# Kernel optimization log

Measured on AMD Instinct MI355X. Metric: run time of the kernel, lower is better.

## Reference

```python
import jax, jax.numpy as jnp
import numpy as np

EPS = 1e-5
MIN_NORM = 1e-10

def _norm(x):
    return jnp.sqrt(jnp.clip(jnp.sum(x * x, axis=-1, keepdims=True), MIN_NORM, None))

def _proj(x):
    # clip points to the open unit Poincare ball
    n = _norm(x)
    max_n = 1.0 - EPS
    return jnp.where(n > max_n, x * (max_n / n), x)

def _artanh(x):
    return jnp.arctanh(jnp.clip(x, -1.0 + EPS, 1.0 - EPS))

def mob_add(u, v):
    uv = jnp.sum(u * v, axis=-1, keepdims=True)
    u2 = jnp.sum(u * u, axis=-1, keepdims=True)
    v2 = jnp.sum(v * v, axis=-1, keepdims=True)
    num = (1.0 + 2.0 * uv + v2) * u + (1.0 - u2) * v
    den = 1.0 + 2.0 * uv + u2 * v2
    return _proj(num / jnp.maximum(den, MIN_NORM))

def mob_mat_mul(M, x):
    # M: [Din, Dout], x: [B, Din] on the ball. Ganea Mobius matvec.
    x = _proj(x)
    Mx = x @ M
    x_n = _norm(x)
    Mx_n = _norm(Mx)
    return _proj(jnp.tanh(Mx_n / x_n * _artanh(x_n)) * (Mx / Mx_n))

def log_map_zero(y):
    n = _norm(y)
    return _artanh(n) * y / n

def exp_map_zero(v):
    n = _norm(v)
    return _proj(jnp.tanh(n) * v / n)

def mob_pointwise_prod(x, u):
    # coordinate-wise scale of hyperbolic x by gate u, in the tangent space at 0
    return exp_map_zero(log_map_zero(x) * u)

def _transition(W, h, U, x, b):
    Wh = mob_mat_mul(W, h)
    Ux = mob_mat_mul(U, x)
    return mob_add(mob_add(Wh, Ux), b)

def setup_inputs() -> dict:
    B, I, H = 2048, 1024, 1024
    Din, Dh = 2 * I, 2 * H
    k = (1.0 / H) ** 0.5
    key = jax.random.key(0)
    ks = jax.random.split(key, 8)
    return {
        "hyp_x": jax.random.normal(ks[0], (B, Din), jnp.float32) * 0.01,
        "hidden": jax.random.normal(ks[1], (B, Dh), jnp.float32) * 0.01,
        "w_z": jax.random.uniform(ks[2], (Dh, Dh), jnp.float32, -k, k),
        "w_r": jax.random.uniform(ks[3], (Dh, Dh), jnp.float32, -k, k),
        "w_h": jax.random.uniform(ks[4], (Dh, Dh), jnp.float32, -k, k),
        "u_z": jax.random.uniform(ks[5], (Din, Dh), jnp.float32, -k, k),
        "u_r": jax.random.uniform(ks[6], (Din, Dh), jnp.float32, -k, k),
        "b_z": jnp.zeros((Dh,), jnp.float32),
        "b_r": jnp.zeros((Dh,), jnp.float32),
        "b_h": jnp.zeros((Dh,), jnp.float32),
    }

def reference(hyp_x, hidden, w_z, w_r, w_h, u_z, u_r, b_z, b_r, b_h):
    hyp_x = _proj(hyp_x)
    hidden = _proj(hidden)
    z = jax.nn.sigmoid(log_map_zero(_transition(w_z, hidden, u_z, hyp_x, b_z)))
    r = jax.nn.sigmoid(log_map_zero(_transition(w_r, hidden, u_r, hyp_x, b_r)))
    r_point_h = mob_pointwise_prod(hidden, r)
    # NOTE: original source uses u_r (not u_h) here; replicated faithfully.
    h_tilde = _transition(w_h, r_point_h, u_r, hyp_x, b_h)
    minus_h_oplus_htilde = mob_add(-hidden, h_tilde)
    new_h = mob_add(hidden, mob_pointwise_prod(minus_h_oplus_htilde, z))
    return new_h
```

## Files before the change

### kernel.cpp

```cpp
#include <hip/hip_runtime.h>
#include <hip/hip_bf16.h>
#include <math.h>

#define EPS 1e-5f
#define MAXN (1.0f - EPS)
#define MINN 1e-10f

constexpr int D = 2048;

typedef unsigned short u16;
typedef __bf16 bf16x8 __attribute__((ext_vector_type(8)));
typedef float floatx4 __attribute__((ext_vector_type(4)));


__device__ __forceinline__ u16 f2bf(float f) {
    union { float f; unsigned u; } v; v.f = f;
    unsigned r = v.u + 0x7FFFu + ((v.u >> 16) & 1u);
    return (u16)(r >> 16);
}

__device__ __forceinline__ float bf2f(u16 b) {
    union { unsigned u; float f; } v; v.u = ((unsigned)b) << 16; return v.f;
}

__device__ __forceinline__ void load_bf8(const u16* p, float* d) {
    uint4 r = *(const uint4*)p;
    unsigned w[4] = {r.x, r.y, r.z, r.w};
    #pragma unroll
    for (int i = 0; i < 4; ++i) {
        d[2 * i]     = bf2f((u16)(w[i] & 0xFFFFu));
        d[2 * i + 1] = bf2f((u16)(w[i] >> 16));
    }
}

__device__ __forceinline__ void store_bf8(u16* p, const float* s) {
    u16 pk[8];
    #pragma unroll
    for (int i = 0; i < 8; ++i) pk[i] = f2bf(s[i]);
    *(uint4*)p = *(const uint4*)pk;
}

__device__ __forceinline__ void load_f8(const float* p, float* d) {
    *(float4*)(d)     = *(const float4*)(p);
    *(float4*)(d + 4) = *(const float4*)(p + 4);
}

__device__ __forceinline__ void store_f8(float* p, const float* s) {
    *(float4*)(p)     = *(const float4*)(s);
    *(float4*)(p + 4) = *(const float4*)(s + 4);
}

__device__ __forceinline__ float artanh_(float x) {
    x = fminf(fmaxf(x, -1.0f + EPS), 1.0f - EPS);
    return 0.5f * logf((1.0f + x) / (1.0f - x));
}

__device__ __forceinline__ float sigmoid_(float x) {
    return 1.0f / (1.0f + expf(-x));
}

__device__ __forceinline__ void gl_lds16(const u16* g, u16* l) {
    __builtin_amdgcn_global_load_lds(
        (const __attribute__((address_space(1))) unsigned int*)g,
        (__attribute__((address_space(3))) unsigned int*)l, 16, 0, 0);
}

template<int N>
__device__ __forceinline__ void block_sums(float* v, float* sbuf) {
    #pragma unroll
    for (int n = 0; n < N; ++n)
        #pragma unroll
        for (int off = 32; off >= 1; off >>= 1) v[n] += __shfl_xor(v[n], off, 64);
    int w = threadIdx.x >> 6;
    __syncthreads();
    if ((threadIdx.x & 63) == 0) {
        #pragma unroll
        for (int n = 0; n < N; ++n) sbuf[w * N + n] = v[n];
    }
    __syncthreads();
    #pragma unroll
    for (int n = 0; n < N; ++n)
        v[n] = sbuf[n] + sbuf[N + n] + sbuf[2 * N + n] + sbuf[3 * N + n];
}

__device__ __forceinline__ void mmm_finish(float sum2, float g, float* coef, float* onorm) {
    float mxn = sqrtf(fmaxf(sum2, MINN));
    float tt  = tanhf(mxn * g);
    float on  = fminf(tt, MAXN);
    *coef = on / mxn;
    *onorm = on;
}

__device__ __forceinline__ float mob_apply(float* u, const float* v,
                                           float u2, float v2, float duv) {
    float cu  = 1.f + 2.f * duv + v2;
    float cv  = 1.f - u2;
    float den = fmaxf(1.f + 2.f * duv + u2 * v2, MINN);
    float s2  = cu * cu * u2 + 2.f * cu * cv * duv + cv * cv * v2;
    float n   = sqrtf(fmaxf(s2 / (den * den), MINN));
    float sc  = ((n > MAXN) ? MAXN / n : 1.f) / den;
    #pragma unroll
    for (int i = 0; i < 8; ++i) u[i] = sc * (cu * u[i] + cv * v[i]);
    return fminf(n, MAXN);
}

__device__ __forceinline__ void trans_tile(const float* W, u16* Wt,
                                           int n0, int k0, float* tile) {
    int t = threadIdx.x;
    int lr = t >> 4, lc = (t & 15) * 4;
    #pragma unroll
    for (int p = 0; p < 4; ++p) {
        int r = lr + p * 16;
        float4 v = *(const float4*)(W + (size_t)(k0 + r) * D + n0 + lc);
        tile[r * 65 + lc + 0] = v.x;
        tile[r * 65 + lc + 1] = v.y;
        tile[r * 65 + lc + 2] = v.z;
        tile[r * 65 + lc + 3] = v.w;
    }
    __syncthreads();
    int wn = t >> 3, ws = (t & 7) * 8;
    #pragma unroll
    for (int p = 0; p < 2; ++p) {
        int n = wn + p * 32;
        u16 pk[8];
        #pragma unroll
        for (int j = 0; j < 8; ++j) pk[j] = f2bf(tile[(ws + j) * 65 + n]);
        *(uint4*)(Wt + (size_t)(n0 + n) * D + k0 + ws) = *(uint4*)pk;
    }
}


struct PrepBatch {
    const float* W[5]; u16* Wt[5];
    const float* hx; const float* h;
    u16* hx_bf; u16* h_bf;
    float* g_x; float* g_h;
};

__global__ __launch_bounds__(256) void wtrans_prep(PrepBatch pb) {
    __shared__ float tile[64 * 65];
    int t = threadIdx.x;

    if (blockIdx.z != 4) {
        int wi = (blockIdx.z == 5) ? 4 : blockIdx.z;
        trans_tile(pb.W[wi], pb.Wt[wi],
                   blockIdx.x * 64, blockIdx.y * 64, tile);
    } else {
        int bid = blockIdx.y * (D / 64) + blockIdx.x;
        for (int rr = 0; rr < 2; ++rr) {
            int b = bid * 2 + rr;
            size_t off = (size_t)b * D + t * 8;
            float xv[8], hv[8];
            load_f8(pb.hx + off, xv);
            load_f8(pb.h + off, hv);
            float s[2] = {0.f, 0.f};
            #pragma unroll
            for (int i = 0; i < 8; ++i) { s[0] += xv[i] * xv[i]; s[1] += hv[i] * hv[i]; }
            block_sums<2>(s, tile);

            float nx = sqrtf(fmaxf(s[0], MINN));
            float scx = (nx > MAXN) ? MAXN / nx : 1.0f;
            float nh = sqrtf(fmaxf(s[1], MINN));
            float sch = (nh > MAXN) ? MAXN / nh : 1.0f;
            #pragma unroll
            for (int i = 0; i < 8; ++i) { xv[i] *= scx; hv[i] *= sch; }
            store_bf8(pb.hx_bf + off, xv);
            store_bf8(pb.h_bf + off, hv);
            if (t == 0) {
                float xn = fminf(nx, MAXN), hn = fminf(nh, MAXN);
                pb.g_x[b] = artanh_(xn) / xn;
                pb.g_h[b] = artanh_(hn) / hn;
            }
        }
    }
}


#define PHASE_MID() do { \
    __builtin_amdgcn_s_barrier(); \
    asm volatile("s_waitcnt lgkmcnt(0)" ::: "memory"); \
    __builtin_amdgcn_sched_barrier(0); \
    __builtin_amdgcn_s_setprio(1); } while (0)

#define PHASE_END() do { \
    __builtin_amdgcn_s_setprio(0); \
    __builtin_amdgcn_s_barrier(); } while (0)

template<int KLEN, int NJ>
__device__ __forceinline__ void gemm256_body(const u16* __restrict__ A,
                                             const u16* __restrict__ W,
                                             u16* __restrict__ C, int koff,
                                             u16* As, u16* Ws) {
    constexpr int T  = KLEN / 64;
    constexpr int BN = NJ * 64;
    constexpr int AU = 8192;
    constexpr int BU = BN * 32;

    int t0 = threadIdx.x;
    int wave = t0 >> 6, lane = t0 & 63, l16 = lane & 15, quad = lane >> 4;
    int wr = wave >> 2, wc = wave & 3;
    int brow = blockIdx.y * 256, bcol = blockIdx.x * BN;

    int srow = t0 >> 2;
    int sseg = (t0 & 3) ^ ((srow >> 1) & 3);
    const u16* srcA = A + (size_t)(brow + srow) * D + koff + sseg * 8;
    const u16* srcB = W + (size_t)(bcol + srow) * D + koff + sseg * 8;
    u16* ldsA = As + wave * 512;
    u16* ldsB = Ws + wave * 512;

    auto stageA = [&](int buf, int kh, int tile) {
        const u16* s = srcA + tile * 64 + kh * 32;
        u16* d = ldsA + (buf * 2 + kh) * AU;
        gl_lds16(s, d);
        gl_lds16(s + (size_t)128 * D, d + 4096);
    };
    auto stageB = [&](int buf, int kh, int tile) {
        const u16* s = srcB + tile * 64 + kh * 32;
        u16* d = ldsB + (buf * 2 + kh) * BU;
        gl_lds16(s, d);
        if constexpr (NJ == 4) gl_lds16(s + (size_t)128 * D, d + 4096);
    };

    const u16* aF = As + (wr * 128 + l16) * 32 + ((quad ^ ((l16 >> 1) & 3)) * 8);
    const u16* bF = Ws + (wc * (NJ * 16) + l16) * 32 + ((quad ^ ((l16 >> 1) & 3)) * 8);

    floatx4 acc[8][NJ];
    #pragma unroll
    for (int i = 0; i < 8; ++i)
        #pragma unroll
        for (int j = 0; j < NJ; ++j)
            #pragma unroll
            for (int e = 0; e < 4; ++e) acc[i][j][e] = 0.f;

    stageA(0, 0, 0); stageB(0, 0, 0);
    stageA(0, 1, 0); stageB(0, 1, 0);
    stageA(1, 0, 1); stageB(1, 0, 1);
    if constexpr (NJ == 4) asm volatile("s_waitcnt vmcnt(4)" ::: "memory");
    else                   asm volatile("s_waitcnt vmcnt(3)" ::: "memory");
    __builtin_amdgcn_s_barrier();

    #pragma unroll 2
    for (int tt = 0; tt < T; ++tt) {
        int bsel = tt & 1, bno = bsel ^ 1;
        const u16* aT = aF + bsel * (2 * AU);
        const u16* bT = bF + bsel * (2 * BU);
        bool st1 = (tt + 1) < T, st2 = (tt + 2) < T;

        if constexpr (NJ == 4) {
            bf16x8 bfr[4], afr[4];
            #pragma unroll
            for (int j = 0; j < 4; ++j) bfr[j] = *(const bf16x8*)(bT + j * 512);
            #pragma unroll
            for (int i = 0; i < 4; ++i) afr[i] = *(const bf16x8*)(aT + i * 512);
            if (st1) stageA(bno, 1, tt + 1);
            PHASE_MID();
            #pragma unroll
            for (int i = 0; i < 4; ++i)
                #pragma unroll
                for (int j = 0; j < 4; ++j)
                    acc[i][j] = __builtin_amdgcn_mfma_f32_16x16x32_bf16(afr[i], bfr[j], acc[i][j], 0, 0, 0);
            PHASE_END();
            #pragma unroll
            for (int i = 0; i < 4; ++i) afr[i] = *(const bf16x8*)(aT + (4 + i) * 512);
            if (st1) stageB(bno, 1, tt + 1);
            PHASE_MID();
            #pragma unroll
            for (int i = 0; i < 4; ++i)
                #pragma unroll
                for (int j = 0; j < 4; ++j)
                    acc[4 + i][j] = __builtin_amdgcn_mfma_f32_16x16x32_bf16(afr[i], bfr[j], acc[4 + i][j], 0, 0, 0);
            PHASE_END();
            #pragma unroll
            for (int j = 0; j < 4; ++j) bfr[j] = *(const bf16x8*)(bT + BU + j * 512);
            #pragma unroll
            for (int i = 0; i < 4; ++i) afr[i] = *(const bf16x8*)(aT + AU + i * 512);
            if (st2) stageA(bsel, 0, tt + 2);
            PHASE_MID();
            #pragma unroll
            for (int i = 0; i < 4; ++i)
                #pragma unroll
                for (int j = 0; j < 4; ++j)
                    acc[i][j] = __builtin_amdgcn_mfma_f32_16x16x32_bf16(afr[i], bfr[j], acc[i][j], 0, 0, 0);
            PHASE_END();
            #pragma unroll
            for (int i = 0; i < 4; ++i) afr[i] = *(const bf16x8*)(aT + AU + (4 + i) * 512);
            if (st2) stageB(bsel, 0, tt + 2);
            PHASE_MID();
            #pragma unroll
            for (int i = 0; i < 4; ++i)
                #pragma unroll
                for (int j = 0; j < 4; ++j)
                    acc[4 + i][j] = __builtin_amdgcn_mfma_f32_16x16x32_bf16(afr[i], bfr[j], acc[4 + i][j], 0, 0, 0);
            __builtin_amdgcn_s_setprio(0);
            asm volatile("s_waitcnt vmcnt(4)" ::: "memory");
            __builtin_amdgcn_s_barrier();
        } else {
            bf16x8 bfr[2], afr[8];
            #pragma unroll
            for (int j = 0; j < 2; ++j) bfr[j] = *(const bf16x8*)(bT + j * 512);
            #pragma unroll
            for (int i = 0; i < 8; ++i) afr[i] = *(const bf16x8*)(aT + i * 512);
            if (st1) { stageA(bno, 1, tt + 1); stageB(bno, 1, tt + 1); }
            PHASE_MID();
            #pragma unroll
            for (int i = 0; i < 8; ++i)
                #pragma unroll
                for (int j = 0; j < 2; ++j)
                    acc[i][j] = __builtin_amdgcn_mfma_f32_16x16x32_bf16(afr[i], bfr[j], acc[i][j], 0, 0, 0);
            PHASE_END();
            #pragma unroll
            for (int j = 0; j < 2; ++j) bfr[j] = *(const bf16x8*)(bT + BU + j * 512);
            #pragma unroll
            for (int i = 0; i < 8; ++i) afr[i] = *(const bf16x8*)(aT + AU + i * 512);
            if (st2) { stageA(bsel, 0, tt + 2); stageB(bsel, 0, tt + 2); }
            PHASE_MID();
            #pragma unroll
            for (int i = 0; i < 8; ++i)
                #pragma unroll
                for (int j = 0; j < 2; ++j)
                    acc[i][j] = __builtin_amdgcn_mfma_f32_16x16x32_bf16(afr[i], bfr[j], acc[i][j], 0, 0, 0);
            __builtin_amdgcn_s_setprio(0);
            asm volatile("s_waitcnt vmcnt(3)" ::: "memory");
            __builtin_amdgcn_s_barrier();
        }
    }

    #pragma unroll
    for (int i = 0; i < 8; ++i) {
        #pragma unroll
        for (int j = 0; j < NJ; ++j) {
            int row = brow + wr * 128 + i * 16 + quad * 4;
            int col = bcol + wc * (NJ * 16) + j * 16 + l16;
            #pragma unroll
            for (int r = 0; r < 4; ++r)
                C[(size_t)(row + r) * D + col] = f2bf(acc[i][j][r]);
        }
    }
}


struct G1Batch { const u16* A[4]; const u16* W[4]; u16* C[4]; };

__global__ __launch_bounds__(512, 2) void g1_kernel(G1Batch gb) {
    __shared__ u16 As[32768];
    __shared__ u16 Ws[32768];
    int z = blockIdx.z;
    gemm256_body<2048, 4>(gb.A[z], gb.W[z], gb.C[z], 0, As, Ws);
}


struct GemmBatch { const u16* A[2]; const u16* W[2]; u16* C[2]; int koff[2]; };

__global__ __launch_bounds__(512, 2) void g2_kernel(GemmBatch gb) {
    __shared__ u16 As[32768];
    __shared__ u16 Ws[16384];
    int z = blockIdx.z;
    gemm256_body<1024, 2>(gb.A[z], gb.W[z], gb.C[z], gb.koff[z], As, Ws);
}


__global__ __launch_bounds__(256) void mid_kernel(
    const u16* __restrict__ c_wz, const u16* __restrict__ c_uz,
    const u16* __restrict__ c_wr, const u16* __restrict__ c_ur,
    const u16* __restrict__ h_bf,
    const float* __restrict__ g_x, const float* __restrict__ g_h,
    const float* __restrict__ b_z, const float* __restrict__ b_r,
    u16* __restrict__ z_out, u16* __restrict__ uxr_out,
    u16* __restrict__ rph_bf, float* __restrict__ g_rph) {
    __shared__ float sbuf[24];
    int b = blockIdx.x, t = threadIdx.x;
    size_t off = (size_t)b * D + t * 8;
    int cbase = t * 8;

    float wz[8], uz[8], wr2[8], ur2[8], hp[8], bz[8], br[8];
    load_bf8(c_wz + off, wz);
    load_bf8(c_uz + off, uz);
    load_bf8(c_wr + off, wr2);
    load_bf8(c_ur + off, ur2);
    load_bf8(h_bf + off, hp);
    load_f8(b_z + cbase, bz);
    load_f8(b_r + cbase, br);

    float s[6] = {0, 0, 0, 0, 0, 0};
    #pragma unroll
    for (int i = 0; i < 8; ++i) {
        s[0] += wz[i] * wz[i];  s[1] += uz[i] * uz[i];
        s[2] += wr2[i] * wr2[i]; s[3] += ur2[i] * ur2[i];
        s[4] += bz[i] * bz[i];  s[5] += br[i] * br[i];
    }
    block_sums<6>(s, sbuf);
    float gh = g_h[b], gx = g_x[b];

    float cwz, nwz, cuz, nuz, cwr, nwr, cur, nur;
    mmm_finish(s[0], gh, &cwz, &nwz);
    mmm_finish(s[1], gx, &cuz, &nuz);
    mmm_finish(s[2], gh, &cwr, &nwr);
    mmm_finish(s[3], gx, &cur, &nur);
    #pragma unroll
    for (int i = 0; i < 8; ++i) {
        wz[i] *= cwz; uz[i] *= cuz; wr2[i] *= cwr; ur2[i] *= cur;
    }
    float sbz = s[4], sbr2 = s[5];

    float d[2] = {0.f, 0.f};
    #pragma unroll
    for (int i = 0; i < 8; ++i) { d[0] += wz[i] * uz[i]; d[1] += wr2[i] * ur2[i]; }
    block_sums<2>(d, sbuf);
    float n1z = mob_apply(wz, uz, nwz * nwz, nuz * nuz, d[0]);
    float n1r = mob_apply(wr2, ur2, nwr * nwr, nur * nur, d[1]);

    d[0] = 0.f; d[1] = 0.f;
    #pragma unroll
    for (int i = 0; i < 8; ++i) { d[0] += wz[i] * bz[i]; d[1] += wr2[i] * br[i]; }
    block_sums<2>(d, sbuf);
    float n2z = mob_apply(wz, bz, n1z * n1z, sbz, d[0]);
    float n2r = mob_apply(wr2, br, n1r * n1r, sbr2, d[1]);

    float gz = artanh_(n2z) / n2z;
    float gr = artanh_(n2r) / n2r;
    float zz[8], v[8];
    float sv = 0.f;
    #pragma unroll
    for (int i = 0; i < 8; ++i) {
        zz[i] = sigmoid_(gz * wz[i]);
        float r = sigmoid_(gr * wr2[i]);
        v[i] = gh * hp[i] * r;
        sv += v[i] * v[i];
    }
    store_bf8(z_out + off, zz);
    block_sums<1>(&sv, sbuf);
    float nv = sqrtf(fmaxf(sv, MINN));
    float th = fminf(tanhf(nv), MAXN);
    float cr = th / nv;
    #pragma unroll
    for (int i = 0; i < 8; ++i) v[i] *= cr;
    store_bf8(rph_bf + off, v);
    store_bf8(uxr_out + off, ur2);
    if (t == 0) g_rph[b] = artanh_(th) / th;
}


__global__ __launch_bounds__(256) void fin_kernel(
    const u16* __restrict__ p0, const u16* __restrict__ p1,
    const u16* __restrict__ uxr, const u16* __restrict__ z_in,
    const u16* __restrict__ h_bf,
    const float* __restrict__ g_rph, const float* __restrict__ b_h,
    float* __restrict__ out) {
    __shared__ float sbuf[16];
    int b = blockIdx.x, t = threadIdx.x;
    size_t off = (size_t)b * D + t * 8;
    int cbase = t * 8;

    float wh[8], ux[8], zz[8], hp[8], bh[8], t0[8];
    load_bf8(p0 + off, wh);
    load_bf8(p1 + off, t0);
    #pragma unroll
    for (int i = 0; i < 8; ++i) wh[i] += t0[i];
    load_bf8(uxr + off, ux);
    load_bf8(z_in + off, zz);
    load_bf8(h_bf + off, hp);
    load_f8(b_h + cbase, bh);

    float s[4] = {0, 0, 0, 0};
    #pragma unroll
    for (int i = 0; i < 8; ++i) {
        s[0] += wh[i] * wh[i]; s[1] += ux[i] * ux[i];
        s[2] += hp[i] * hp[i]; s[3] += bh[i] * bh[i];
    }
    block_sums<4>(s, sbuf);
    float swh = s[0], sux = s[1], shp = s[2], sbh = s[3];

    float cwh, nwh;
    mmm_finish(swh, g_rph[b], &cwh, &nwh);
    #pragma unroll
    for (int i = 0; i < 8; ++i) wh[i] *= cwh;

    float d = 0.f;
    #pragma unroll
    for (int i = 0; i < 8; ++i) d += wh[i] * ux[i];
    block_sums<1>(&d, sbuf);
    float n1 = mob_apply(wh, ux, nwh * nwh, sux, d);

    d = 0.f;
    #pragma unroll
    for (int i = 0; i < 8; ++i) d += wh[i] * bh[i];
    block_sums<1>(&d, sbuf);
    float nht = mob_apply(wh, bh, n1 * n1, sbh, d);

    #pragma unroll
    for (int i = 0; i < 8; ++i) ux[i] = -hp[i];
    d = 0.f;
    #pragma unroll
    for (int i = 0; i < 8; ++i) d += ux[i] * wh[i];
    block_sums<1>(&d, sbuf);
    float nm = mob_apply(ux, wh, shp, nht * nht, d);

    float lm = artanh_(nm) / nm;
    float sv = 0.f;
    #pragma unroll
    for (int i = 0; i < 8; ++i) {
        float v = lm * ux[i] * zz[i];
        ux[i] = v;
        sv += v * v;
    }
    block_sums<1>(&sv, sbuf);
    float nv = sqrtf(fmaxf(sv, MINN));
    float th = fminf(tanhf(nv), MAXN);
    float ce = th / nv;
    #pragma unroll
    for (int i = 0; i < 8; ++i) ux[i] *= ce;

    d = 0.f;
    #pragma unroll
    for (int i = 0; i < 8; ++i) d += hp[i] * ux[i];
    block_sums<1>(&d, sbuf);
    mob_apply(hp, ux, shp, th * th, d);
    store_f8(out + off, hp);
}


extern "C" void kernel_launch(void* const* d_in, const int* in_sizes, int n_in,
                              void* d_out, int out_size, void* d_ws, size_t ws_size,
                              hipStream_t stream) {
    const float* hyp_x  = (const float*)d_in[0];
    const float* hidden = (const float*)d_in[1];
    const float* w_z = (const float*)d_in[2];
    const float* w_r = (const float*)d_in[3];
    const float* w_h = (const float*)d_in[4];
    const float* u_z = (const float*)d_in[5];
    const float* u_r = (const float*)d_in[6];
    const float* b_z = (const float*)d_in[7];
    const float* b_r = (const float*)d_in[8];
    const float* b_h = (const float*)d_in[9];
    float* out = (float*)d_out;

    int B = in_sizes[1] / D;

    char* ws = (char*)d_ws;
    size_t o = 0;
    auto alloc = [&](size_t bytes) -> void* {
        void* p = ws + o;
        o += (bytes + 255) & ~(size_t)255;
        return p;
    };
    u16* wt[5];
    for (int i = 0; i < 5; ++i) wt[i] = (u16*)alloc((size_t)D * D * 2);
    u16* hx_bf = (u16*)alloc((size_t)B * D * 2);
    u16* h_bf  = (u16*)alloc((size_t)B * D * 2);
    float* g_x   = (float*)alloc((size_t)B * 4);
    float* g_h   = (float*)alloc((size_t)B * 4);
    float* g_rph = (float*)alloc((size_t)B * 4);
    u16* cz0 = (u16*)alloc((size_t)B * D * 2);
    u16* cz1 = (u16*)alloc((size_t)B * D * 2);
    u16* cz2 = (u16*)alloc((size_t)B * D * 2);
    u16* cz3 = (u16*)alloc((size_t)B * D * 2);
    u16* p0 = (u16*)alloc((size_t)B * D * 2);
    u16* p1 = (u16*)alloc((size_t)B * D * 2);
    u16* z_buf = (u16*)alloc((size_t)B * D * 2);
    u16* uxr = (u16*)alloc((size_t)B * D * 2);
    u16* rph = (u16*)alloc((size_t)B * D * 2);

    PrepBatch pb;
    pb.W[0] = w_z; pb.Wt[0] = wt[0];
    pb.W[1] = w_r; pb.Wt[1] = wt[1];
    pb.W[2] = u_z; pb.Wt[2] = wt[3];
    pb.W[3] = u_r; pb.Wt[3] = wt[4];
    pb.W[4] = w_h; pb.Wt[4] = wt[2];
    pb.hx = hyp_x; pb.h = hidden;
    pb.hx_bf = hx_bf; pb.h_bf = h_bf;
    pb.g_x = g_x; pb.g_h = g_h;
    wtrans_prep<<<dim3(D / 64, D / 64, 6), 256, 0, stream>>>(pb);

    G1Batch g1;
    g1.A[0] = h_bf;  g1.W[0] = wt[0]; g1.C[0] = cz0;
    g1.A[1] = hx_bf; g1.W[1] = wt[3]; g1.C[1] = cz1;
    g1.A[2] = h_bf;  g1.W[2] = wt[1]; g1.C[2] = cz2;
    g1.A[3] = hx_bf; g1.W[3] = wt[4]; g1.C[3] = cz3;
    g1_kernel<<<dim3(D / 256, B / 256, 4), 512, 0, stream>>>(g1);

    mid_kernel<<<dim3(B), 256, 0, stream>>>(cz0, cz1, cz2, cz3, h_bf, g_x, g_h,
                                            b_z, b_r, z_buf, uxr, rph, g_rph);

    GemmBatch g2;
    g2.A[0] = rph; g2.W[0] = wt[2]; g2.C[0] = p0; g2.koff[0] = 0;
    g2.A[1] = rph; g2.W[1] = wt[2]; g2.C[1] = p1; g2.koff[1] = 1024;
    g2_kernel<<<dim3(D / 128, B / 256, 2), 512, 0, stream>>>(g2);

    fin_kernel<<<dim3(B), 256, 0, stream>>>(p0, p1, uxr, z_buf, h_bf,
                                            g_rph, b_h, out);
}
```

Baseline: 296.4 us.

## Double-buffer LDS fragment registers so MFMA overlaps next-phase LDS reads

Restructures the GEMM main loop to keep two sets of A/B fragment registers. The next phase's LDS fragment reads are issued before the current phase's MFMA block, and the first fragments of the following tile are loaded at the end of each iteration. This aims to hide LDS read latency behind matrix-core work instead of stalling on lgkmcnt before each MFMA batch. It costs more VGPRs, which can lower occupancy or cause spills, and it reorders the barriers.

```diff
diff --git a/kernel.cpp b/kernel.cpp
--- a/kernel.cpp
+++ b/kernel.cpp
@@ -176,15 +176,15 @@
 }
 
 
-#define PHASE_MID() do { \
-    __builtin_amdgcn_s_barrier(); \
+#define LGKM0_SB() do { \
     asm volatile("s_waitcnt lgkmcnt(0)" ::: "memory"); \
+    __builtin_amdgcn_sched_barrier(0); } while (0)
+
+#define MFMA_BEGIN() do { \
     __builtin_amdgcn_sched_barrier(0); \
     __builtin_amdgcn_s_setprio(1); } while (0)
 
-#define PHASE_END() do { \
-    __builtin_amdgcn_s_setprio(0); \
-    __builtin_amdgcn_s_barrier(); } while (0)
+#define MFMA_END() __builtin_amdgcn_s_setprio(0)
 
 template<int KLEN, int NJ>
 __device__ __forceinline__ void gemm256_body(const u16* __restrict__ A,
@@ -239,89 +239,133 @@
     else                   asm volatile("s_waitcnt vmcnt(3)" ::: "memory");
     __builtin_amdgcn_s_barrier();
 
-    #pragma unroll 2
-    for (int tt = 0; tt < T; ++tt) {
-        int bsel = tt & 1, bno = bsel ^ 1;
-        const u16* aT = aF + bsel * (2 * AU);
-        const u16* bT = bF + bsel * (2 * BU);
-        bool st1 = (tt + 1) < T, st2 = (tt + 2) < T;
-
-        if constexpr (NJ == 4) {
-            bf16x8 bfr[4], afr[4];
-            #pragma unroll
-            for (int j = 0; j < 4; ++j) bfr[j] = *(const bf16x8*)(bT + j * 512);
-            #pragma unroll
-            for (int i = 0; i < 4; ++i) afr[i] = *(const bf16x8*)(aT + i * 512);
+    if constexpr (NJ == 4) {
+        bf16x8 fA0[4], fA1[4], fB0[4], fB1[4];
+        #pragma unroll
+        for (int i = 0; i < 4; ++i) fA0[i] = *(const bf16x8*)(aF + i * 512);
+        #pragma unroll
+        for (int j = 0; j < 4; ++j) fB0[j] = *(const bf16x8*)(bF + j * 512);
+
+        #pragma unroll 2
+        for (int tt = 0; tt < T; ++tt) {
+            int bsel = tt & 1, bno = bsel ^ 1;
+            const u16* aT = aF + bsel * (2 * AU);
+            const u16* bT = bF + bsel * (2 * BU);
+            const u16* aN = aF + bno * (2 * AU);
+            const u16* bN = bF + bno * (2 * BU);
+            bool st1 = (tt + 1) < T, st2 = (tt + 2) < T;
+
+            __builtin_amdgcn_s_barrier();
+            LGKM0_SB();
+            #pragma unroll
+            for (int i = 0; i < 4; ++i) fA1[i] = *(const bf16x8*)(aT + (4 + i) * 512);
             if (st1) stageA(bno, 1, tt + 1);
-            PHASE_MID();
+            MFMA_BEGIN();
             #pragma unroll
             for (int i = 0; i < 4; ++i)
                 #pragma unroll
                 for (int j = 0; j < 4; ++j)
-                    acc[i][j] = __builtin_amdgcn_mfma_f32_16x16x32_bf16(afr[i], bfr[j], acc[i][j], 0, 0, 0);
-            PHASE_END();
-            #pragma unroll
-            for (int i = 0; i < 4; ++i) afr[i] = *(const bf16x8*)(aT + (4 + i) * 512);
+                    acc[i][j] = __builtin_amdgcn_mfma_f32_16x16x32_bf16(fA0[i], fB0[j], acc[i][j], 0, 0, 0);
+            MFMA_END();
+
+            __builtin_amdgcn_s_barrier();
+            LGKM0_SB();
+            #pragma unroll
+            for (int i = 0; i < 4; ++i) fA0[i] = *(const bf16x8*)(aT + AU + i * 512);
+            #pragma unroll
+            for (int j = 0; j < 4; ++j) fB1[j] = *(const bf16x8*)(bT + BU + j * 512);
             if (st1) stageB(bno, 1, tt + 1);
-            PHASE_MID();
+            MFMA_BEGIN();
             #pragma unroll
             for (int i = 0; i < 4; ++i)
                 #pragma unroll
                 for (int j = 0; j < 4; ++j)
-                    acc[4 + i][j] = __builtin_amdgcn_mfma_f32_16x16x32_bf16(afr[i], bfr[j], acc[4 + i][j], 0, 0, 0);
-            PHASE_END();
-            #pragma unroll
-            for (int j = 0; j < 4; ++j) bfr[j] = *(const bf16x8*)(bT + BU + j * 512);
-            #pragma unroll
-            for (int i = 0; i < 4; ++i) afr[i] = *(const bf16x8*)(aT + AU + i * 512);
+                    acc[4 + i][j] = __builtin_amdgcn_mfma_f32_16x16x32_bf16(fA1[i], fB0[j], acc[4 + i][j], 0, 0, 0);
+            MFMA_END();
+
+            __builtin_amdgcn_s_barrier();
+            LGKM0_SB();
+            #pragma unroll
+            for (int i = 0; i < 4; ++i) fA1[i] = *(const bf16x8*)(aT + AU + (4 + i) * 512);
             if (st2) stageA(bsel, 0, tt + 2);
-            PHASE_MID();
+            MFMA_BEGIN();
             #pragma unroll
             for (int i = 0; i < 4; ++i)
                 #pragma unroll
                 for (int j = 0; j < 4; ++j)
-                    acc[i][j] = __builtin_amdgcn_mfma_f32_16x16x32_bf16(afr[i], bfr[j], acc[i][j], 0, 0, 0);
-            PHASE_END();
-            #pragma unroll
-            for (int i = 0; i < 4; ++i) afr[i] = *(const bf16x8*)(aT + AU + (4 + i) * 512);
+                    acc[i][j] = __builtin_amdgcn_mfma_f32_16x16x32_bf16(fA0[i], fB1[j], acc[i][j], 0, 0, 0);
+            MFMA_END();
+
+            __builtin_amdgcn_s_barrier();
+            LGKM0_SB();
             if (st2) stageB(bsel, 0, tt + 2);
-            PHASE_MID();
+            asm volatile("s_waitcnt vmcnt(4)" ::: "memory");
+            __builtin_amdgcn_s_barrier();
+            __builtin_amdgcn_sched_barrier(0);
+            if (st1) {
+                #pragma unroll
+                for (int i = 0; i < 4; ++i) fA0[i] = *(const bf16x8*)(aN + i * 512);
+                #pragma unroll
+                for (int j = 0; j < 4; ++j) fB0[j] = *(const bf16x8*)(bN + j * 512);
+            }
+            MFMA_BEGIN();
             #pragma unroll
             for (int i = 0; i < 4; ++i)
                 #pragma unroll
                 for (int j = 0; j < 4; ++j)
-                    acc[4 + i][j] = __builtin_amdgcn_mfma_f32_16x16x32_bf16(afr[i], bfr[j], acc[4 + i][j], 0, 0, 0);
-            __builtin_amdgcn_s_setprio(0);
-            asm volatile("s_waitcnt vmcnt(4)" ::: "memory");
-            __builtin_amdgcn_s_barrier();
-        } else {
-            bf16x8 bfr[2], afr[8];
-            #pragma unroll
-            for (int j = 0; j < 2; ++j) bfr[j] = *(const bf16x8*)(bT + j * 512);
-            #pragma unroll
-            for (int i = 0; i < 8; ++i) afr[i] = *(const bf16x8*)(aT + i * 512);
+                    acc[4 + i][j] = __builtin_amdgcn_mfma_f32_16x16x32_bf16(fA1[i], fB1[j], acc[4 + i][j], 0, 0, 0);
+            MFMA_END();
+        }
+    } else {
+        bf16x8 fA0[8], fA1[8], fB0[2], fB1[2];
+        #pragma unroll
+        for (int i = 0; i < 8; ++i) fA0[i] = *(const bf16x8*)(aF + i * 512);
+        #pragma unroll
+        for (int j = 0; j < 2; ++j) fB0[j] = *(const bf16x8*)(bF + j * 512);
+
+        #pragma unroll 2
+        for (int tt = 0; tt < T; ++tt) {
+            int bsel = tt & 1, bno = bsel ^ 1;
+            const u16* aT = aF + bsel * (2 * AU);
+            const u16* bT = bF + bsel * (2 * BU);
+            const u16* aN = aF + bno * (2 * AU);
+            const u16* bN = bF + bno * (2 * BU);
+            bool st1 = (tt + 1) < T, st2 = (tt + 2) < T;
+
+            __builtin_amdgcn_s_barrier();
+            LGKM0_SB();
+            #pragma unroll
+            for (int i = 0; i < 8; ++i) fA1[i] = *(const bf16x8*)(aT + AU + i * 512);
+            #pragma unroll
+            for (int j = 0; j < 2; ++j) fB1[j] = *(const bf16x8*)(bT + BU + j * 512);
             if (st1) { stageA(bno, 1, tt + 1); stageB(bno, 1, tt + 1); }
-            PHASE_MID();
+            MFMA_BEGIN();
             #pragma unroll
             for (int i = 0; i < 8; ++i)
                 #pragma unroll
                 for (int j = 0; j < 2; ++j)
-                    acc[i][j] = __builtin_amdgcn_mfma_f32_16x16x32_bf16(afr[i], bfr[j], acc[i][j], 0, 0, 0);
-            PHASE_END();
-            #pragma unroll
-            for (int j = 0; j < 2; ++j) bfr[j] = *(const bf16x8*)(bT + BU + j * 512);
-            #pragma unroll
-            for (int i = 0; i < 8; ++i) afr[i] = *(const bf16x8*)(aT + AU + i * 512);
+                    acc[i][j] = __builtin_amdgcn_mfma_f32_16x16x32_bf16(fA0[i], fB0[j], acc[i][j], 0, 0, 0);
+            MFMA_END();
+
+            __builtin_amdgcn_s_barrier();
+            LGKM0_SB();
             if (st2) { stageA(bsel, 0, tt + 2); stageB(bsel, 0, tt + 2); }
-            PHASE_MID();
+            asm volatile("s_waitcnt vmcnt(3)" ::: "memory");
+            __builtin_amdgcn_s_barrier();
+            __builtin_amdgcn_sched_barrier(0);
+            if (st1) {
+                #pragma unroll
+                for (int i = 0; i < 8; ++i) fA0[i] = *(const bf16x8*)(aN + i * 512);
+                #pragma unroll
+                for (int j = 0; j < 2; ++j) fB0[j] = *(const bf16x8*)(bN + j * 512);
+            }
+            MFMA_BEGIN();
             #pragma unroll
             for (int i = 0; i < 8; ++i)
                 #pragma unroll
                 for (int j = 0; j < 2; ++j)
-                    acc[i][j] = __builtin_amdgcn_mfma_f32_16x16x32_bf16(afr[i], bfr[j], acc[i][j], 0, 0, 0);
-            __builtin_amdgcn_s_setprio(0);
-            asm volatile("s_waitcnt vmcnt(3)" ::: "memory");
-            __builtin_amdgcn_s_barrier();
+                    acc[i][j] = __builtin_amdgcn_mfma_f32_16x16x32_bf16(fA1[i], fB1[j], acc[i][j], 0, 0, 0);
+            MFMA_END();
         }
     }
 
```

After: 318.2 us. 1.07x slower.
